# Kernel tuning notes

Measured on AMD Instinct MI355X. Metric: run time of the kernel, lower is better.

Reference implementation:

```python
import jax, jax.numpy as jnp
import numpy as np

B, T, C, HS = 4, 4096, 1024, 128

def setup_inputs() -> dict:
    key = jax.random.key(0)
    kx, kq, kk, kv = jax.random.split(key, 4)
    x = jax.random.normal(kx, (B, T, C), dtype=jnp.float32)
    # bias-free Linear weights, stored as (in, out) so projection is x @ W
    scale = 1.0 / np.sqrt(C)
    Wq = jax.random.normal(kq, (C, HS), dtype=jnp.float32) * scale
    Wk = jax.random.normal(kk, (C, HS), dtype=jnp.float32) * scale
    Wv = jax.random.normal(kv, (C, HS), dtype=jnp.float32) * scale
    return {"x": x, "Wq": Wq, "Wk": Wk, "Wv": Wv}

def reference(x, Wq, Wk, Wv):
    # x: (B,T,C) -> q,k,v: (B,T,HS)
    q = jnp.einsum('btc,ch->bth', x, Wq)
    k = jnp.einsum('btc,ch->bth', x, Wk)
    v = jnp.einsum('btc,ch->bth', x, Wv)
    hs = k.shape[-1]
    # scaled scores (B,T,T) with causal mask
    wei = jnp.einsum('bth,bsh->bts', q, k) * (hs ** -0.5)
    causal = jnp.tril(jnp.ones((q.shape[1], q.shape[1]), dtype=bool))
    wei = jnp.where(causal, wei, -jnp.inf)
    wei = jax.nn.softmax(wei, axis=-1)
    # dropout p=0.0 -> identity
    out = jnp.einsum('bts,bsh->bth', wei, v)
    return out
```

## Files before the change

### kernel.cpp

```cpp
#include <hip/hip_runtime.h>
#include <hip/hip_bf16.h>

typedef __attribute__((ext_vector_type(8))) short short8;
typedef __attribute__((ext_vector_type(4))) short s4v;
typedef __attribute__((ext_vector_type(4))) float f32x4;

#define BATCH 4
#define TLEN 4096
#define CDIM 1024
#define HSD 128
#define MROWS (BATCH*TLEN)

#define QSCALE 0.12751744f

#ifdef __HIP_DEVICE_COMPILE__
  #define MFMA16(a,b,c) __builtin_amdgcn_mfma_f32_16x16x16bf16_1k(a,b,c,0,0,0)
#else
  #define MFMA16(a,b,c) (c)
#endif

__device__ __forceinline__ unsigned short f2bf(float f){
    unsigned u = __builtin_bit_cast(unsigned, f);
    u = (u + 0x7FFFu + ((u >> 16) & 1u)) >> 16;
    return (unsigned short)u;
}
__device__ __forceinline__ unsigned pkbf(float a, float b){
    unsigned ua = (__builtin_bit_cast(unsigned, a) + 0x8000u) >> 16;
    unsigned ub = (__builtin_bit_cast(unsigned, b) + 0x8000u) & 0xFFFF0000u;
    return ua | ub;
}

__global__ void prep_w_k(const float* __restrict__ Wq, const float* __restrict__ Wk,
                         const float* __restrict__ Wv, unsigned short* __restrict__ Wt){
    int idx = blockIdx.x * 256 + threadIdx.x;
    const int total = 3 * HSD * CDIM;
    if (idx >= total) return;
    int w = idx / (HSD * CDIM);
    int r = idx - w * HSD * CDIM;
    int h = r / CDIM;
    int c = r - h * CDIM;
    const float* W = (w == 0) ? Wq : ((w == 1) ? Wk : Wv);
    Wt[idx] = f2bf(W[c * HSD + h]);
}

__device__ __forceinline__ void stage_w_tile(unsigned short* buf, const unsigned short* g,
                                             int tid){
#pragma unroll
    for (int i = 0; i < 2; i++){
        int c = i * 256 + tid;
        int row = c >> 2, kp = c & 3;
        int swz = (row & 3) ^ ((row >> 2) & 3);
        const unsigned short* gp = g + (size_t)row * CDIM + ((kp ^ swz) << 3);
        unsigned short* lp = buf + (c << 3);
        __builtin_amdgcn_global_load_lds((const __attribute__((address_space(1))) void*)gp,
                                         (__attribute__((address_space(3))) void*)lp, 16, 0, 0);
    }
}

__global__ __launch_bounds__(256) void proj_k(const float* __restrict__ x,
                                              const unsigned short* __restrict__ Wt,
                                              unsigned short* __restrict__ Qb,
                                              unsigned short* __restrict__ Kb,
                                              unsigned short* __restrict__ Vt){
    __shared__ unsigned short As[2][64 * 32];
    __shared__ unsigned short Bs[2][128 * 32];

    const int tid = threadIdx.x, lane = tid & 63, wave = tid >> 6;
    const int m = lane & 15, quad = lane >> 4;
    const int wr = wave & 1, wc = wave >> 1;
    const int rb = blockIdx.x * 64;
    const int p  = blockIdx.y;

    const float* gA = x + (size_t)rb * CDIM;
    const unsigned short* gB = Wt + (size_t)(p * HSD) * CDIM;

    const int arow = tid >> 2, ach = tid & 3;
    const int aswz = (arow & 3) ^ ((arow >> 2) & 3);
    const int agc = ach ^ aswz;
    const float* agp = gA + (size_t)arow * CDIM + (agc << 3);

    f32x4 acc[4][4];
#pragma unroll
    for (int i = 0; i < 4; i++)
#pragma unroll
        for (int j = 0; j < 4; j++) acc[i][j] = (f32x4)0.f;

    stage_w_tile(&Bs[0][0], gB, tid);
    {
        float4 a0 = *(const float4*)(agp);
        float4 a1 = *(const float4*)(agp + 4);
        short8 o;
        o[0]=(short)f2bf(a0.x); o[1]=(short)f2bf(a0.y); o[2]=(short)f2bf(a0.z); o[3]=(short)f2bf(a0.w);
        o[4]=(short)f2bf(a1.x); o[5]=(short)f2bf(a1.y); o[6]=(short)f2bf(a1.z); o[7]=(short)f2bf(a1.w);
        *(short8*)&As[0][arow * 32 + (ach << 3)] = o;
    }
    __syncthreads();

    int cur = 0;
    for (int kc = 0; kc < CDIM / 32; ++kc){
        float4 a0n, a1n;
        if (kc + 1 < CDIM / 32){
            stage_w_tile(&Bs[cur ^ 1][0], gB + (kc + 1) * 32, tid);
            a0n = *(const float4*)(agp + (kc + 1) * 32);
            a1n = *(const float4*)(agp + (kc + 1) * 32 + 4);
        }
        if (p < 2){
            short8 aF[4], bF[2];
#pragma unroll
            for (int i = 0; i < 4; i++){
                int ra = wr * 64 + i * 16 + m;
                int sa = (ra & 3) ^ ((ra >> 2) & 3);
                aF[i] = *(const short8*)&Bs[cur][ra * 32 + ((quad ^ sa) << 3)];
            }
#pragma unroll
            for (int j = 0; j < 2; j++){
                int rn = wc * 32 + j * 16 + m;
                int sb = (rn & 3) ^ ((rn >> 2) & 3);
                bF[j] = *(const short8*)&As[cur][rn * 32 + ((quad ^ sb) << 3)];
            }
#pragma unroll
            for (int i = 0; i < 4; i++)
#pragma unroll
                for (int j = 0; j < 2; j++)
                    acc[i][j] = __builtin_amdgcn_mfma_f32_16x16x32_bf16(aF[i], bF[j], acc[i][j], 0, 0, 0);
        } else {
            short8 aF[2], bF[4];
#pragma unroll
            for (int i = 0; i < 2; i++){
                int ra = wr * 32 + i * 16 + m;
                int sa = (ra & 3) ^ ((ra >> 2) & 3);
                aF[i] = *(const short8*)&As[cur][ra * 32 + ((quad ^ sa) << 3)];
            }
#pragma unroll
            for (int j = 0; j < 4; j++){
                int rn = wc * 64 + j * 16 + m;
                int sb = (rn & 3) ^ ((rn >> 2) & 3);
                bF[j] = *(const short8*)&Bs[cur][rn * 32 + ((quad ^ sb) << 3)];
            }
#pragma unroll
            for (int i = 0; i < 2; i++)
#pragma unroll
                for (int j = 0; j < 4; j++)
                    acc[i][j] = __builtin_amdgcn_mfma_f32_16x16x32_bf16(aF[i], bF[j], acc[i][j], 0, 0, 0);
        }
        if (kc + 1 < CDIM / 32){
            short8 o;
            o[0]=(short)f2bf(a0n.x); o[1]=(short)f2bf(a0n.y); o[2]=(short)f2bf(a0n.z); o[3]=(short)f2bf(a0n.w);
            o[4]=(short)f2bf(a1n.x); o[5]=(short)f2bf(a1n.y); o[6]=(short)f2bf(a1n.z); o[7]=(short)f2bf(a1n.w);
            *(short8*)&As[cur ^ 1][arow * 32 + (ach << 3)] = o;
        }
        __syncthreads();
        cur ^= 1;
    }

    if (p < 2){
        unsigned short* D = (p == 0) ? Qb : Kb;
        const float qs = (p == 0) ? QSCALE : 1.0f;
#pragma unroll
        for (int i = 0; i < 4; i++){
#pragma unroll
            for (int j = 0; j < 2; j++){
                int h = wr * 64 + i * 16 + quad * 4;
                int t = rb + wc * 32 + j * 16 + m;
                ushort4 v;
                v.x = f2bf(acc[i][j][0] * qs); v.y = f2bf(acc[i][j][1] * qs);
                v.z = f2bf(acc[i][j][2] * qs); v.w = f2bf(acc[i][j][3] * qs);
                *(ushort4*)(D + (size_t)t * HSD + h) = v;
            }
        }
    } else {
        int b = rb >> 12;
        int tb = rb & 4095;
#pragma unroll
        for (int i = 0; i < 2; i++){
#pragma unroll
            for (int j = 0; j < 4; j++){
                int t = tb + wr * 32 + i * 16 + quad * 4;
                int h = wc * 64 + j * 16 + m;
                ushort4 v;
                v.x = f2bf(acc[i][j][0]); v.y = f2bf(acc[i][j][1]);
                v.z = f2bf(acc[i][j][2]); v.w = f2bf(acc[i][j][3]);
                *(ushort4*)(Vt + ((size_t)b * HSD + h) * TLEN + t) = v;
            }
        }
    }
}

__device__ __forceinline__ void stage_k_tile(unsigned short* buf, const unsigned short* g,
                                             int tid){
#pragma unroll
    for (int i = 0; i < 2; i++){
        int slot = i * 512 + tid;
        int row = slot >> 4;
        int ch  = slot & 15;
        const unsigned short* gp = g + row * 128 + ((ch ^ (row & 15)) << 3);
        unsigned short* lp = buf + (slot << 3);
        __builtin_amdgcn_global_load_lds((const __attribute__((address_space(1))) void*)gp,
                                         (__attribute__((address_space(3))) void*)lp, 16, 0, 0);
    }
}
__device__ __forceinline__ void stage_v_tile(unsigned short* buf, const unsigned short* g,
                                             int tid){
#pragma unroll
    for (int i = 0; i < 2; i++){
        int slot = i * 512 + tid;
        int row = slot >> 3;
        int ch  = slot & 7;
        const unsigned short* gp = g + (size_t)row * TLEN + ((ch ^ (row & 7)) << 3);
        unsigned short* lp = buf + (slot << 3);
        __builtin_amdgcn_global_load_lds((const __attribute__((address_space(1))) void*)gp,
                                         (__attribute__((address_space(3))) void*)lp, 16, 0, 0);
    }
}

__global__ __launch_bounds__(512) void attn_k(const unsigned short* __restrict__ Qb,
                       const unsigned short* __restrict__ Kb,
                       const unsigned short* __restrict__ Vts,
                       float* __restrict__ Opart, float* __restrict__ lpart, int seglen){
    __shared__ unsigned short Kt[64 * 128];
    __shared__ unsigned short Vs[128 * 64];

    const int tid = threadIdx.x, lane = tid & 63, wave = tid >> 6;
    const int m = lane & 15, quad = lane >> 4;
    const int q0 = ((int)gridDim.x - 1 - (int)blockIdx.x) * 128;
    const int seg = blockIdx.y, b = blockIdx.z;
    const int g0 = seg * seglen;
    if (g0 >= q0 + 128) return;
    const int gend = min(g0 + seglen, q0 + 128);
    const int nT = (gend - g0) >> 6;

    const int q0w = q0 + wave * 16;
    const size_t rowg = (size_t)b * TLEN + q0w;

    short8 aQ[4];
#pragma unroll
    for (int kk = 0; kk < 4; kk++)
        aQ[kk] = *(const short8*)(Qb + (rowg + m) * HSD + kk * 32 + quad * 8);

    f32x4 accO[8];
#pragma unroll
    for (int i = 0; i < 8; i++) accO[i] = (f32x4)0.f;
    float lp = 0.f;

    const unsigned short* kbase = Kb + (size_t)b * TLEN * HSD;
    const unsigned short* vbase = Vts + (size_t)b * HSD * TLEN;

    for (int t = 0; t < nT; ++t){
        const int s0 = g0 + t * 64;
        stage_k_tile(&Kt[0], kbase + (size_t)s0 * HSD, tid);
        stage_v_tile(&Vs[0], vbase + s0, tid);
        __syncthreads();

        if (s0 <= q0w + 15){
            f32x4 S[4];
#pragma unroll
            for (int ns = 0; ns < 4; ns++){
                f32x4 sa = (f32x4)0.f;
#pragma unroll
                for (int kk = 0; kk < 4; kk++){
                    short8 bK = *(const short8*)&Kt[(ns * 16 + m) * 128 + (((kk * 4 + quad) ^ m) << 3)];
                    sa = __builtin_amdgcn_mfma_f32_16x16x32_bf16(bK, aQ[kk], sa, 0, 0, 0);
                }
                S[ns] = sa;
            }
            if (s0 + 63 > q0w){
                int qg = q0w + m;
#pragma unroll
                for (int ns = 0; ns < 4; ns++){
#pragma unroll
                    for (int r = 0; r < 4; r++){
                        int sg = s0 + ns * 16 + quad * 4 + r;
                        if (sg > qg) S[ns][r] = -1e30f;
                    }
                }
            }
            s4v aP[4];
#pragma unroll
            for (int ns = 0; ns < 4; ns++){
                float p0 = exp2f(S[ns][0]), p1 = exp2f(S[ns][1]);
                float p2 = exp2f(S[ns][2]), p3 = exp2f(S[ns][3]);
                lp += (p0 + p1) + (p2 + p3);
                uint2 u;
                u.x = pkbf(p0, p1);
                u.y = pkbf(p2, p3);
                aP[ns] = __builtin_bit_cast(s4v, u);
            }
#pragma unroll
            for (int sub = 0; sub < 8; sub++){
#pragma unroll
                for (int ns = 0; ns < 4; ns++){
                    s4v bV = *(const s4v*)&Vs[(sub * 16 + m) * 64 +
                            (((2 * ns + (quad >> 1)) ^ (m & 7)) << 3) + (quad & 1) * 4];
                    accO[sub] = MFMA16(aP[ns], bV, accO[sub]);
                }
            }
        }
        __syncthreads();
    }
    lp += __shfl_xor(lp, 16, 64);
    lp += __shfl_xor(lp, 32, 64);
    if (quad == 0)
        lpart[(size_t)seg * MROWS + rowg + m] = lp;
    float* ob = Opart + (size_t)seg * MROWS * HSD;
#pragma unroll
    for (int sub = 0; sub < 8; sub++)
#pragma unroll
        for (int r = 0; r < 4; r++)
            ob[(rowg + quad * 4 + r) * HSD + sub * 16 + m] = accO[sub][r];
}

__global__ void merge_k(const float* __restrict__ Opart, const float* __restrict__ lpart,
                        float* __restrict__ out, int nseg, int seglen){
    int idx = blockIdx.x * 256 + threadIdx.x;
    int row = idx >> 7;
    int t = row & (TLEN - 1);
    int q0 = t & ~127;
    int nsv = min(nseg, (q0 + 127) / seglen + 1);
    float L = 0.f, o = 0.f;
    for (int s = 0; s < nsv; s++){
        L += lpart[(size_t)s * MROWS + row];
        o += Opart[(size_t)s * MROWS * HSD + idx];
    }
    out[idx] = o / L;
}

extern "C" void kernel_launch(void* const* d_in, const int* in_sizes, int n_in,
                              void* d_out, int out_size, void* d_ws, size_t ws_size,
                              hipStream_t stream) {
    const float* x  = (const float*)d_in[0];
    const float* Wq = (const float*)d_in[1];
    const float* Wk = (const float*)d_in[2];
    const float* Wv = (const float*)d_in[3];
    float* out = (float*)d_out;
    char* w = (char*)d_ws;

    unsigned short* Wt = (unsigned short*)w;
    unsigned short* Qb = (unsigned short*)(w + ((size_t)1u  << 20));
    unsigned short* Kb = (unsigned short*)(w + ((size_t)5u  << 20));
    unsigned short* Vt = (unsigned short*)(w + ((size_t)9u  << 20));
    float* lpart       = (float*)(w + ((size_t)13u << 20));
    float* Opart;
    int nseg;
    const size_t segbytes = (size_t)MROWS * HSD * 4;
    if (ws_size >= ((size_t)14u << 20) + 8 * segbytes){
        nseg = 8;  Opart = (float*)(w + ((size_t)14u << 20));
    } else if (ws_size >= ((size_t)14u << 20) + 4 * segbytes){
        nseg = 4;  Opart = (float*)(w + ((size_t)14u << 20));
    } else {
        nseg = 1;  Opart = out;
    }
    const int seglen = TLEN / nseg;

    prep_w_k<<<(3 * HSD * CDIM + 255) / 256, 256, 0, stream>>>(Wq, Wk, Wv, Wt);
    proj_k<<<dim3(MROWS / 64, 3), 256, 0, stream>>>(x, Wt, Qb, Kb, Vt);
    attn_k<<<dim3(TLEN / 128, nseg, BATCH), 512, 0, stream>>>(Qb, Kb, Vt, Opart, lpart, seglen);
    merge_k<<<(MROWS * HSD) / 256, 256, 0, stream>>>(Opart, lpart, out, nseg, seglen);
}
```

Baseline: 201.9 us.

## Give each attention wave 32 query rows and pre-swizzle K/V into fragment-ordered LDS

The attention kernel moves from 512 threads with 16 query rows per wave to 256 threads with 32 rows per wave. Each K and V fragment read from LDS is now reused for two MFMA row blocks, which halves LDS reads per MFMA. K is staged straight into LDS in MFMA-fragment order, so each lane reads with a simple linear offset. V is loaded through registers and scattered into fragment order. The cost is twice the accumulator registers (launch_bounds 256,3), a coarser causal skip granularity, and V staging that no longer goes directly from global memory to LDS.

```diff
diff --git a/kernel.cpp b/kernel.cpp
--- a/kernel.cpp
+++ b/kernel.cpp
@@ -186,39 +186,12 @@
     }
 }
 
-__device__ __forceinline__ void stage_k_tile(unsigned short* buf, const unsigned short* g,
-                                             int tid){
-#pragma unroll
-    for (int i = 0; i < 2; i++){
-        int slot = i * 512 + tid;
-        int row = slot >> 4;
-        int ch  = slot & 15;
-        const unsigned short* gp = g + row * 128 + ((ch ^ (row & 15)) << 3);
-        unsigned short* lp = buf + (slot << 3);
-        __builtin_amdgcn_global_load_lds((const __attribute__((address_space(1))) void*)gp,
-                                         (__attribute__((address_space(3))) void*)lp, 16, 0, 0);
-    }
-}
-__device__ __forceinline__ void stage_v_tile(unsigned short* buf, const unsigned short* g,
-                                             int tid){
-#pragma unroll
-    for (int i = 0; i < 2; i++){
-        int slot = i * 512 + tid;
-        int row = slot >> 3;
-        int ch  = slot & 7;
-        const unsigned short* gp = g + (size_t)row * TLEN + ((ch ^ (row & 7)) << 3);
-        unsigned short* lp = buf + (slot << 3);
-        __builtin_amdgcn_global_load_lds((const __attribute__((address_space(1))) void*)gp,
-                                         (__attribute__((address_space(3))) void*)lp, 16, 0, 0);
-    }
-}
-
-__global__ __launch_bounds__(512) void attn_k(const unsigned short* __restrict__ Qb,
+__global__ __launch_bounds__(256, 3) void attn_k(const unsigned short* __restrict__ Qb,
                        const unsigned short* __restrict__ Kb,
                        const unsigned short* __restrict__ Vts,
                        float* __restrict__ Opart, float* __restrict__ lpart, int seglen){
-    __shared__ unsigned short Kt[64 * 128];
-    __shared__ unsigned short Vs[128 * 64];
+    __shared__ unsigned short Kf[16 * 512];
+    __shared__ unsigned short Vf[32 * 256];
 
     const int tid = threadIdx.x, lane = tid & 63, wave = tid >> 6;
     const int m = lane & 15, quad = lane >> 4;
@@ -229,84 +202,128 @@
     const int gend = min(g0 + seglen, q0 + 128);
     const int nT = (gend - g0) >> 6;
 
-    const int q0w = q0 + wave * 16;
+    const int q0w = q0 + wave * 32;
     const size_t rowg = (size_t)b * TLEN + q0w;
 
-    short8 aQ[4];
-#pragma unroll
-    for (int kk = 0; kk < 4; kk++)
-        aQ[kk] = *(const short8*)(Qb + (rowg + m) * HSD + kk * 32 + quad * 8);
-
-    f32x4 accO[8];
-#pragma unroll
-    for (int i = 0; i < 8; i++) accO[i] = (f32x4)0.f;
-    float lp = 0.f;
+    short8 aQ[2][4];
+#pragma unroll
+    for (int h = 0; h < 2; h++)
+#pragma unroll
+        for (int kk = 0; kk < 4; kk++)
+            aQ[h][kk] = *(const short8*)(Qb + (rowg + h * 16 + m) * HSD + kk * 32 + quad * 8);
+
+    f32x4 accO[2][8];
+#pragma unroll
+    for (int h = 0; h < 2; h++)
+#pragma unroll
+        for (int i = 0; i < 8; i++) accO[h][i] = (f32x4)0.f;
+    float lp0 = 0.f, lp1 = 0.f;
 
     const unsigned short* kbase = Kb + (size_t)b * TLEN * HSD;
     const unsigned short* vbase = Vts + (size_t)b * HSD * TLEN;
 
+    int koff[4];
+#pragma unroll
+    for (int i = 0; i < 4; i++){
+        int s = i * 256 + tid;
+        int g = s >> 6, l = s & 63;
+        int ns = g >> 2, kk = g & 3, qd = l >> 4, mm = l & 15;
+        koff[i] = (16 * ns + mm) * HSD + kk * 32 + qd * 8;
+    }
+    int voff[4], vdst[4];
+#pragma unroll
+    for (int i = 0; i < 4; i++){
+        int c = i * 256 + tid;
+        int mm = c & 15, sc = (c >> 4) & 7, hi = c >> 7;
+        voff[i] = (hi * 16 + mm) * TLEN + sc * 8;
+        int ns = sc >> 1, qa = (sc & 1) * 2;
+        vdst[i] = ((hi * 4 + ns) * 64 + qa * 16 + mm) * 4;
+    }
+
+    const unsigned short* kl = Kf + lane * 8;
+    const unsigned short* vl = Vf + lane * 4;
+
     for (int t = 0; t < nT; ++t){
         const int s0 = g0 + t * 64;
-        stage_k_tile(&Kt[0], kbase + (size_t)s0 * HSD, tid);
-        stage_v_tile(&Vs[0], vbase + s0, tid);
+        const unsigned short* kt = kbase + (size_t)s0 * HSD;
+#pragma unroll
+        for (int i = 0; i < 4; i++){
+            __builtin_amdgcn_global_load_lds(
+                (const __attribute__((address_space(1))) void*)(kt + koff[i]),
+                (__attribute__((address_space(3))) void*)(Kf + (size_t)(i * 256 + tid) * 8),
+                16, 0, 0);
+        }
+        uint4 vv[4];
+#pragma unroll
+        for (int i = 0; i < 4; i++)
+            vv[i] = *(const uint4*)(vbase + voff[i] + s0);
+#pragma unroll
+        for (int i = 0; i < 4; i++){
+            *(uint2*)&Vf[vdst[i]]      = make_uint2(vv[i].x, vv[i].y);
+            *(uint2*)&Vf[vdst[i] + 64] = make_uint2(vv[i].z, vv[i].w);
+        }
         __syncthreads();
 
-        if (s0 <= q0w + 15){
-            f32x4 S[4];
+        if (s0 <= q0w + 31){
+            s4v aP[2][4];
 #pragma unroll
             for (int ns = 0; ns < 4; ns++){
-                f32x4 sa = (f32x4)0.f;
-#pragma unroll
-                for (int kk = 0; kk < 4; kk++){
-                    short8 bK = *(const short8*)&Kt[(ns * 16 + m) * 128 + (((kk * 4 + quad) ^ m) << 3)];
-                    sa = __builtin_amdgcn_mfma_f32_16x16x32_bf16(bK, aQ[kk], sa, 0, 0, 0);
+                short8 kf[4];
+#pragma unroll
+                for (int kk = 0; kk < 4; kk++)
+                    kf[kk] = *(const short8*)(kl + (ns * 4 + kk) * 512);
+#pragma unroll
+                for (int h = 0; h < 2; h++){
+                    f32x4 sa = (f32x4)0.f;
+#pragma unroll
+                    for (int kk = 0; kk < 4; kk++)
+                        sa = __builtin_amdgcn_mfma_f32_16x16x32_bf16(kf[kk], aQ[h][kk], sa, 0, 0, 0);
+                    if (s0 + 63 > q0w){
+                        int qg = q0w + h * 16 + m;
+#pragma unroll
+                        for (int r = 0; r < 4; r++){
+                            int sg = s0 + ns * 16 + quad * 4 + r;
+                            if (sg > qg) sa[r] = -1e30f;
+                        }
+                    }
+                    float p0 = exp2f(sa[0]), p1 = exp2f(sa[1]);
+                    float p2 = exp2f(sa[2]), p3 = exp2f(sa[3]);
+                    if (h == 0) lp0 += (p0 + p1) + (p2 + p3);
+                    else        lp1 += (p0 + p1) + (p2 + p3);
+                    uint2 u;
+                    u.x = pkbf(p0, p1);
+                    u.y = pkbf(p2, p3);
+                    aP[h][ns] = __builtin_bit_cast(s4v, u);
                 }
-                S[ns] = sa;
-            }
-            if (s0 + 63 > q0w){
-                int qg = q0w + m;
+            }
+#pragma unroll
+            for (int sub = 0; sub < 8; sub++){
 #pragma unroll
                 for (int ns = 0; ns < 4; ns++){
-#pragma unroll
-                    for (int r = 0; r < 4; r++){
-                        int sg = s0 + ns * 16 + quad * 4 + r;
-                        if (sg > qg) S[ns][r] = -1e30f;
-                    }
+                    s4v bV = *(const s4v*)(vl + (sub * 4 + ns) * 256);
+                    accO[0][sub] = MFMA16(aP[0][ns], bV, accO[0][sub]);
+                    accO[1][sub] = MFMA16(aP[1][ns], bV, accO[1][sub]);
                 }
             }
-            s4v aP[4];
-#pragma unroll
-            for (int ns = 0; ns < 4; ns++){
-                float p0 = exp2f(S[ns][0]), p1 = exp2f(S[ns][1]);
-                float p2 = exp2f(S[ns][2]), p3 = exp2f(S[ns][3]);
-                lp += (p0 + p1) + (p2 + p3);
-                uint2 u;
-                u.x = pkbf(p0, p1);
-                u.y = pkbf(p2, p3);
-                aP[ns] = __builtin_bit_cast(s4v, u);
-            }
-#pragma unroll
-            for (int sub = 0; sub < 8; sub++){
-#pragma unroll
-                for (int ns = 0; ns < 4; ns++){
-                    s4v bV = *(const s4v*)&Vs[(sub * 16 + m) * 64 +
-                            (((2 * ns + (quad >> 1)) ^ (m & 7)) << 3) + (quad & 1) * 4];
-                    accO[sub] = MFMA16(aP[ns], bV, accO[sub]);
-                }
-            }
         }
         __syncthreads();
     }
-    lp += __shfl_xor(lp, 16, 64);
-    lp += __shfl_xor(lp, 32, 64);
-    if (quad == 0)
-        lpart[(size_t)seg * MROWS + rowg + m] = lp;
+    lp0 += __shfl_xor(lp0, 16, 64);
+    lp0 += __shfl_xor(lp0, 32, 64);
+    lp1 += __shfl_xor(lp1, 16, 64);
+    lp1 += __shfl_xor(lp1, 32, 64);
+    if (quad == 0){
+        lpart[(size_t)seg * MROWS + rowg + m]      = lp0;
+        lpart[(size_t)seg * MROWS + rowg + 16 + m] = lp1;
+    }
     float* ob = Opart + (size_t)seg * MROWS * HSD;
 #pragma unroll
-    for (int sub = 0; sub < 8; sub++)
-#pragma unroll
-        for (int r = 0; r < 4; r++)
-            ob[(rowg + quad * 4 + r) * HSD + sub * 16 + m] = accO[sub][r];
+    for (int h = 0; h < 2; h++)
+#pragma unroll
+        for (int sub = 0; sub < 8; sub++)
+#pragma unroll
+            for (int r = 0; r < 4; r++)
+                ob[(rowg + h * 16 + quad * 4 + r) * HSD + sub * 16 + m] = accO[h][sub][r];
 }
 
 __global__ void merge_k(const float* __restrict__ Opart, const float* __restrict__ lpart,
@@ -353,6 +370,6 @@
 
     prep_w_k<<<(3 * HSD * CDIM + 255) / 256, 256, 0, stream>>>(Wq, Wk, Wv, Wt);
     proj_k<<<dim3(MROWS / 64, 3), 256, 0, stream>>>(x, Wt, Qb, Kb, Vt);
-    attn_k<<<dim3(TLEN / 128, nseg, BATCH), 512, 0, stream>>>(Qb, Kb, Vt, Opart, lpart, seglen);
+    attn_k<<<dim3(TLEN / 128, nseg, BATCH), 256, 0, stream>>>(Qb, Kb, Vt, Opart, lpart, seglen);
     merge_k<<<(MROWS * HSD) / 256, 256, 0, stream>>>(Opart, lpart, out, nseg, seglen);
 }
```

After: 209.9 us. 1.04x slower.

## Store K/V tiles in MFMA fragment order and use bf16 partial outputs

Applied to the files above, without the earlier changes.

K tiles are now staged into LDS in the exact per-lane MFMA fragment order, so the fragment reads become contiguous lane-strided loads without XOR swizzle math. V tiles are loaded through registers and scattered into fragment order. The score, mask and exp steps are fused per 16-column slice, and __launch_bounds__ adds a minimum-occupancy hint of 2. Partial outputs are stored as bf16 instead of fp32, which halves the traffic written by attn_k and read by merge_k at the cost of extra rounding, and the nseg=1 path now also goes through the workspace.

```diff
diff --git a/kernel.cpp b/kernel.cpp
--- a/kernel.cpp
+++ b/kernel.cpp
@@ -186,39 +186,13 @@
     }
 }
 
-__device__ __forceinline__ void stage_k_tile(unsigned short* buf, const unsigned short* g,
-                                             int tid){
-#pragma unroll
-    for (int i = 0; i < 2; i++){
-        int slot = i * 512 + tid;
-        int row = slot >> 4;
-        int ch  = slot & 15;
-        const unsigned short* gp = g + row * 128 + ((ch ^ (row & 15)) << 3);
-        unsigned short* lp = buf + (slot << 3);
-        __builtin_amdgcn_global_load_lds((const __attribute__((address_space(1))) void*)gp,
-                                         (__attribute__((address_space(3))) void*)lp, 16, 0, 0);
-    }
-}
-__device__ __forceinline__ void stage_v_tile(unsigned short* buf, const unsigned short* g,
-                                             int tid){
-#pragma unroll
-    for (int i = 0; i < 2; i++){
-        int slot = i * 512 + tid;
-        int row = slot >> 3;
-        int ch  = slot & 7;
-        const unsigned short* gp = g + (size_t)row * TLEN + ((ch ^ (row & 7)) << 3);
-        unsigned short* lp = buf + (slot << 3);
-        __builtin_amdgcn_global_load_lds((const __attribute__((address_space(1))) void*)gp,
-                                         (__attribute__((address_space(3))) void*)lp, 16, 0, 0);
-    }
-}
-
-__global__ __launch_bounds__(512) void attn_k(const unsigned short* __restrict__ Qb,
+__global__ __launch_bounds__(512, 2) void attn_k(const unsigned short* __restrict__ Qb,
                        const unsigned short* __restrict__ Kb,
                        const unsigned short* __restrict__ Vts,
-                       float* __restrict__ Opart, float* __restrict__ lpart, int seglen){
-    __shared__ unsigned short Kt[64 * 128];
-    __shared__ unsigned short Vs[128 * 64];
+                       unsigned short* __restrict__ Opart, float* __restrict__ lpart,
+                       int seglen){
+    __shared__ unsigned short Kf[16 * 512];
+    __shared__ unsigned short Vf[32 * 256];
 
     const int tid = threadIdx.x, lane = tid & 63, wave = tid >> 6;
     const int m = lane & 15, quad = lane >> 4;
@@ -245,40 +219,66 @@
     const unsigned short* kbase = Kb + (size_t)b * TLEN * HSD;
     const unsigned short* vbase = Vts + (size_t)b * HSD * TLEN;
 
+    int koff[2], voff[2], vdst[2];
+#pragma unroll
+    for (int i = 0; i < 2; i++){
+        int s = i * 512 + tid;
+        int g = s >> 6, l = s & 63;
+        int ns = g >> 2, kk = g & 3, qd = l >> 4, mm = l & 15;
+        koff[i] = (16 * ns + mm) * HSD + kk * 32 + qd * 8;
+        int c = i * 512 + tid;
+        int vm = c & 15, sc = (c >> 4) & 7, hi = c >> 7;
+        voff[i] = (hi * 16 + vm) * TLEN + sc * 8;
+        int vns = sc >> 1, qa = (sc & 1) * 2;
+        vdst[i] = ((hi * 4 + vns) * 64 + qa * 16 + vm) * 4;
+    }
+    const unsigned short* kl = Kf + lane * 8;
+    const unsigned short* vl = Vf + lane * 4;
+
     for (int t = 0; t < nT; ++t){
         const int s0 = g0 + t * 64;
-        stage_k_tile(&Kt[0], kbase + (size_t)s0 * HSD, tid);
-        stage_v_tile(&Vs[0], vbase + s0, tid);
+        const unsigned short* kt = kbase + (size_t)s0 * HSD;
+#pragma unroll
+        for (int i = 0; i < 2; i++){
+            __builtin_amdgcn_global_load_lds(
+                (const __attribute__((address_space(1))) void*)(kt + koff[i]),
+                (__attribute__((address_space(3))) void*)(Kf + (size_t)(i * 512 + tid) * 8),
+                16, 0, 0);
+        }
+        uint4 vv[2];
+#pragma unroll
+        for (int i = 0; i < 2; i++)
+            vv[i] = *(const uint4*)(vbase + voff[i] + s0);
+#pragma unroll
+        for (int i = 0; i < 2; i++){
+            *(uint2*)&Vf[vdst[i]]      = make_uint2(vv[i].x, vv[i].y);
+            *(uint2*)&Vf[vdst[i] + 64] = make_uint2(vv[i].z, vv[i].w);
+        }
         __syncthreads();
 
         if (s0 <= q0w + 15){
-            f32x4 S[4];
+            s4v aP[4];
 #pragma unroll
             for (int ns = 0; ns < 4; ns++){
+                short8 kf0 = *(const short8*)(kl + (ns * 4 + 0) * 512);
+                short8 kf1 = *(const short8*)(kl + (ns * 4 + 1) * 512);
+                short8 kf2 = *(const short8*)(kl + (ns * 4 + 2) * 512);
+                short8 kf3 = *(const short8*)(kl + (ns * 4 + 3) * 512);
                 f32x4 sa = (f32x4)0.f;
-#pragma unroll
-                for (int kk = 0; kk < 4; kk++){
-                    short8 bK = *(const short8*)&Kt[(ns * 16 + m) * 128 + (((kk * 4 + quad) ^ m) << 3)];
-                    sa = __builtin_amdgcn_mfma_f32_16x16x32_bf16(bK, aQ[kk], sa, 0, 0, 0);
-                }
-                S[ns] = sa;
-            }
-            if (s0 + 63 > q0w){
-                int qg = q0w + m;
-#pragma unroll
-                for (int ns = 0; ns < 4; ns++){
+                sa = __builtin_amdgcn_mfma_f32_16x16x32_bf16(kf0, aQ[0], sa, 0, 0, 0);
+                sa = __builtin_amdgcn_mfma_f32_16x16x32_bf16(kf1, aQ[1], sa, 0, 0, 0);
+                sa = __builtin_amdgcn_mfma_f32_16x16x32_bf16(kf2, aQ[2], sa, 0, 0, 0);
+                sa = __builtin_amdgcn_mfma_f32_16x16x32_bf16(kf3, aQ[3], sa, 0, 0, 0);
+                if (s0 + 63 > q0w){
+                    int qg = q0w + m;
 #pragma unroll
                     for (int r = 0; r < 4; r++){
                         int sg = s0 + ns * 16 + quad * 4 + r;
-                        if (sg > qg) S[ns][r] = -1e30f;
+                        if (sg > qg) sa[r] = -1e30f;
                     }
                 }
-            }
-            s4v aP[4];
-#pragma unroll
-            for (int ns = 0; ns < 4; ns++){
-                float p0 = exp2f(S[ns][0]), p1 = exp2f(S[ns][1]);
-                float p2 = exp2f(S[ns][2]), p3 = exp2f(S[ns][3]);
+                float p0 = exp2f(sa[0]), p1 = exp2f(sa[1]);
+                float p2 = exp2f(sa[2]), p3 = exp2f(sa[3]);
                 lp += (p0 + p1) + (p2 + p3);
                 uint2 u;
                 u.x = pkbf(p0, p1);
@@ -289,8 +289,7 @@
             for (int sub = 0; sub < 8; sub++){
 #pragma unroll
                 for (int ns = 0; ns < 4; ns++){
-                    s4v bV = *(const s4v*)&Vs[(sub * 16 + m) * 64 +
-                            (((2 * ns + (quad >> 1)) ^ (m & 7)) << 3) + (quad & 1) * 4];
+                    s4v bV = *(const s4v*)(vl + (sub * 4 + ns) * 256);
                     accO[sub] = MFMA16(aP[ns], bV, accO[sub]);
                 }
             }
@@ -301,15 +300,16 @@
     lp += __shfl_xor(lp, 32, 64);
     if (quad == 0)
         lpart[(size_t)seg * MROWS + rowg + m] = lp;
-    float* ob = Opart + (size_t)seg * MROWS * HSD;
+    unsigned short* ob = Opart + ((size_t)seg * MROWS + rowg) * HSD;
 #pragma unroll
     for (int sub = 0; sub < 8; sub++)
 #pragma unroll
         for (int r = 0; r < 4; r++)
-            ob[(rowg + quad * 4 + r) * HSD + sub * 16 + m] = accO[sub][r];
-}
-
-__global__ void merge_k(const float* __restrict__ Opart, const float* __restrict__ lpart,
+            ob[(quad * 4 + r) * HSD + sub * 16 + m] = f2bf(accO[sub][r]);
+}
+
+__global__ void merge_k(const unsigned short* __restrict__ Opart,
+                        const float* __restrict__ lpart,
                         float* __restrict__ out, int nseg, int seglen){
     int idx = blockIdx.x * 256 + threadIdx.x;
     int row = idx >> 7;
@@ -319,7 +319,8 @@
     float L = 0.f, o = 0.f;
     for (int s = 0; s < nsv; s++){
         L += lpart[(size_t)s * MROWS + row];
-        o += Opart[(size_t)s * MROWS * HSD + idx];
+        unsigned u = Opart[(size_t)s * MROWS * HSD + idx];
+        o += __builtin_bit_cast(float, u << 16);
     }
     out[idx] = o / L;
 }
@@ -339,16 +340,14 @@
     unsigned short* Kb = (unsigned short*)(w + ((size_t)5u  << 20));
     unsigned short* Vt = (unsigned short*)(w + ((size_t)9u  << 20));
     float* lpart       = (float*)(w + ((size_t)13u << 20));
-    float* Opart;
+    unsigned short* Opart = (unsigned short*)(w + ((size_t)14u << 20));
+
     int nseg;
-    const size_t segbytes = (size_t)MROWS * HSD * 4;
-    if (ws_size >= ((size_t)14u << 20) + 8 * segbytes){
-        nseg = 8;  Opart = (float*)(w + ((size_t)14u << 20));
-    } else if (ws_size >= ((size_t)14u << 20) + 4 * segbytes){
-        nseg = 4;  Opart = (float*)(w + ((size_t)14u << 20));
-    } else {
-        nseg = 1;  Opart = out;
-    }
+    const size_t segbytes = (size_t)MROWS * HSD * 2;
+    if      (ws_size >= ((size_t)14u << 20) + 8 * segbytes) nseg = 8;
+    else if (ws_size >= ((size_t)14u << 20) + 4 * segbytes) nseg = 4;
+    else if (ws_size >= ((size_t)14u << 20) + 2 * segbytes) nseg = 2;
+    else                                                    nseg = 1;
     const int seglen = TLEN / nseg;
 
     prep_w_k<<<(3 * HSD * CDIM + 255) / 256, 256, 0, stream>>>(Wq, Wk, Wv, Wt);
```

After: 203.7 us. No clear change (+0.9%).
